# Kernel optimization log

Hardware: AMD Instinct MI355X
Metric: run time of the kernel (lower is better)

The kernel has to match this reference:

```python
import jax, jax.numpy as jnp
import numpy as np

B, C, H, W = 32, 256, 64, 64
S, K = 128, 8  # NUM_CHANNEL_SETS, MAX_CHANNELS_PER_SET


def setup_inputs() -> dict:
    key = jax.random.key(0)
    kx, ki = jax.random.split(key)
    x = jax.random.normal(kx, (B, C, H, W), dtype=jnp.float32)
    channel_idx_sets = jax.random.randint(ki, (S, K), 0, C, dtype=jnp.int32)
    return {"x": x, "channel_idx_sets": channel_idx_sets}


def reference(x, channel_idx_sets):
    # Gather channels for each set, then max-reduce over the set dimension.
    # x: [B, C, H, W]; channel_idx_sets: [S, K] int32 -> out: [B, S, H, W]
    gathered = x[:, channel_idx_sets, :, :]  # [B, S, K, H, W]
    return jnp.max(gathered, axis=2)
```

## Files before the change

kernel.cpp:

```cpp
#include <hip/hip_runtime.h>


constexpr int Bb = 32, Cc = 256, Hh = 64, Ww = 64, Ss = 128, Kk = 8;
constexpr int HW4 = (Hh * Ww) / 4;
constexpr int T4  = 16;
constexpr int NT  = HW4 / T4;

__global__ __launch_bounds__(256, 2) void fmp_kernel(
    const float4* __restrict__ x4,
    const int*    __restrict__ idx,
    float4*       __restrict__ out4)
{
    __shared__ float4 lx[Cc * T4];
    __shared__ int4   lidx4[Ss * Kk / 4];

    const int tid  = threadIdx.x;
    const int tile = blockIdx.x & (NT - 1);
    const int b    = blockIdx.x >> 6;

    lidx4[tid] = ((const int4*)idx)[tid];

    const float4* __restrict__ xb = x4 + (size_t)b * (Cc * HW4) + tile * T4;
    #pragma unroll
    for (int i = 0; i < 16; ++i) {
        const int flat = i * 256 + tid;
        const int c    = flat >> 4;
        const int tt   = flat & (T4 - 1);
        lx[flat] = xb[(size_t)c * HW4 + tt];
    }
    __syncthreads();

    const int t = tid & (T4 - 1);
    float4* __restrict__ op = out4 + (size_t)b * (Ss * HW4) + tile * T4 + t;

#define FMAX4(m, c) { const float4 v = lx[(c) * T4 + t];          \
        m.x = fmaxf(m.x, v.x); m.y = fmaxf(m.y, v.y);             \
        m.z = fmaxf(m.z, v.z); m.w = fmaxf(m.w, v.w); }

    #pragma unroll
    for (int pass = 0; pass < 8; ++pass) {
        const int s   = pass * 16 + (tid >> 4);
        const int4 i0 = lidx4[s * 2];
        const int4 i1 = lidx4[s * 2 + 1];
        float4 m = lx[i0.x * T4 + t];
        FMAX4(m, i0.y); FMAX4(m, i0.z); FMAX4(m, i0.w);
        FMAX4(m, i1.x); FMAX4(m, i1.y); FMAX4(m, i1.z); FMAX4(m, i1.w);
        op[(size_t)s * HW4] = m;
    }
#undef FMAX4
}

extern "C" void kernel_launch(void* const* d_in, const int* in_sizes, int n_in,
                              void* d_out, int out_size, void* d_ws, size_t ws_size,
                              hipStream_t stream) {
    const float4* x4  = (const float4*)d_in[0];
    const int*    idx = (const int*)d_in[1];
    float4*       o4  = (float4*)d_out;

    const int blocks = Bb * NT;
    fmp_kernel<<<blocks, 256, 0, stream>>>(x4, idx, o4);
}
```

Before: 211.3 us.

## Make blocks persistent over tiles with double-buffered async global-to-LDS loads

Halves the spatial tile width and has each block walk 8 consecutive tiles, launching 512 blocks instead of 2048. Input staging now uses `global_load_lds` direct-to-LDS async copies into two LDS buffers, so the next tile's load is issued before the current tile's max reduction runs. The goal is to overlap global reads with LDS compute and output stores, rather than stalling on a full load before each block's work. In exchange, each channel's contiguous read shrinks to 128 bytes. There is also a full barrier per tile, and the block count is only enough for about one wave across the device.

```diff
diff --git a/kernel.cpp b/kernel.cpp
--- a/kernel.cpp
+++ b/kernel.cpp
@@ -1,51 +1,84 @@
 #include <hip/hip_runtime.h>
+#include <stdint.h>
 
 
 constexpr int Bb = 32, Cc = 256, Hh = 64, Ww = 64, Ss = 128, Kk = 8;
 constexpr int HW4 = (Hh * Ww) / 4;
-constexpr int T4  = 16;
+constexpr int T4  = 8;
 constexpr int NT  = HW4 / T4;
+constexpr int TPB = 8;
+constexpr int NBLK = Bb * NT / TPB;
+
+__device__ __forceinline__ void async_copy16(float4* lds_dst, const float4* g_src) {
+    __builtin_amdgcn_global_load_lds(
+        (const __attribute__((address_space(1))) void*)g_src,
+        (__attribute__((address_space(3))) void*)lds_dst,
+        16, 0, 0);
+}
 
 __global__ __launch_bounds__(256, 2) void fmp_kernel(
     const float4* __restrict__ x4,
     const int*    __restrict__ idx,
     float4*       __restrict__ out4)
 {
-    __shared__ float4 lx[Cc * T4];
+    __shared__ float4 lx[2][Cc * T4];
     __shared__ int4   lidx4[Ss * Kk / 4];
 
-    const int tid  = threadIdx.x;
-    const int tile = blockIdx.x & (NT - 1);
-    const int b    = blockIdx.x >> 6;
+    const int tid   = threadIdx.x;
+    const int b     = blockIdx.x >> 4;
+    const int tile0 = (blockIdx.x & 15) * TPB;
 
     lidx4[tid] = ((const int4*)idx)[tid];
 
-    const float4* __restrict__ xb = x4 + (size_t)b * (Cc * HW4) + tile * T4;
+    const float4* __restrict__ xb = x4 + (size_t)b * (Cc * HW4) + tile0 * T4;
+    const float4* gsrc[8];
     #pragma unroll
-    for (int i = 0; i < 16; ++i) {
+    for (int i = 0; i < 8; ++i) {
         const int flat = i * 256 + tid;
-        const int c    = flat >> 4;
-        const int tt   = flat & (T4 - 1);
-        lx[flat] = xb[(size_t)c * HW4 + tt];
+        gsrc[i] = xb + (size_t)(flat >> 3) * HW4 + (flat & (T4 - 1));
     }
-    __syncthreads();
+    const int wbase = (tid >> 6) * 64;
 
-    const int t = tid & (T4 - 1);
-    float4* __restrict__ op = out4 + (size_t)b * (Ss * HW4) + tile * T4 + t;
+    #pragma unroll
+    for (int i = 0; i < 8; ++i)
+        async_copy16(&lx[0][i * 256 + wbase], gsrc[i]);
 
-#define FMAX4(m, c) { const float4 v = lx[(c) * T4 + t];          \
+    asm volatile("s_waitcnt vmcnt(0) lgkmcnt(0)" ::: "memory");
+    __builtin_amdgcn_s_barrier();
+
+    const int t  = tid & (T4 - 1);
+    const int sg = tid >> 3;
+    float4* __restrict__ op = out4 + (size_t)b * (Ss * HW4) + tile0 * T4 + t;
+
+#define FMAX4(m, c) { const float4 v = L[(c) * T4 + t];           \
         m.x = fmaxf(m.x, v.x); m.y = fmaxf(m.y, v.y);             \
         m.z = fmaxf(m.z, v.z); m.w = fmaxf(m.w, v.w); }
 
     #pragma unroll
-    for (int pass = 0; pass < 8; ++pass) {
-        const int s   = pass * 16 + (tid >> 4);
-        const int4 i0 = lidx4[s * 2];
-        const int4 i1 = lidx4[s * 2 + 1];
-        float4 m = lx[i0.x * T4 + t];
-        FMAX4(m, i0.y); FMAX4(m, i0.z); FMAX4(m, i0.w);
-        FMAX4(m, i1.x); FMAX4(m, i1.y); FMAX4(m, i1.z); FMAX4(m, i1.w);
-        op[(size_t)s * HW4] = m;
+    for (int j = 0; j < TPB; ++j) {
+        const int cur = j & 1;
+
+        if (j + 1 < TPB) {
+            #pragma unroll
+            for (int i = 0; i < 8; ++i)
+                async_copy16(&lx[cur ^ 1][i * 256 + wbase],
+                             gsrc[i] + (size_t)(j + 1) * T4);
+        }
+
+        const float4* __restrict__ L = lx[cur];
+        #pragma unroll
+        for (int pass = 0; pass < 4; ++pass) {
+            const int  s  = pass * 32 + sg;
+            const int4 i0 = lidx4[s * 2];
+            const int4 i1 = lidx4[s * 2 + 1];
+            float4 m = L[i0.x * T4 + t];
+            FMAX4(m, i0.y); FMAX4(m, i0.z); FMAX4(m, i0.w);
+            FMAX4(m, i1.x); FMAX4(m, i1.y); FMAX4(m, i1.z); FMAX4(m, i1.w);
+            op[(size_t)s * HW4 + j * T4] = m;
+        }
+
+        asm volatile("s_waitcnt vmcnt(0)" ::: "memory");
+        __builtin_amdgcn_s_barrier();
     }
 #undef FMAX4
 }
@@ -57,6 +90,5 @@
     const int*    idx = (const int*)d_in[1];
     float4*       o4  = (float4*)d_out;
 
-    const int blocks = Bb * NT;
-    fmp_kernel<<<blocks, 256, 0, stream>>>(x4, idx, o4);
+    fmp_kernel<<<NBLK, 256, 0, stream>>>(x4, idx, o4);
 }
```

Measured after the change: 217.5 us. 2.9% more time.
